# Performance work log

Measured on AMD Instinct MI355X. Metric: run time of the kernel, lower is better.

The kernel has to match this reference:

```python
import jax, jax.numpy as jnp
import numpy as np

N_NODES, N_EDGES, N_GRAPHS, EMB_DIM, IMG_DIM, N_TYPES = 50000, 800000, 64, 128, 4096, 30


def gcn_conv(x, W, b, row, col, ew, dis, n):
    # PyG GCNConv: x @ W.T, symmetric-normalized weighted aggregation with self-loops, + bias
    xw = x @ W.T                                            # [N, D]
    norm = dis[row] * ew * dis[col]                          # [E]
    agg = jax.ops.segment_sum(norm[:, None] * xw[row], col, num_segments=n)
    agg = agg + (dis * dis)[:, None] * xw                    # self-loop (weight 1) term
    return agg + b


def setup_inputs() -> dict:
    key = jax.random.key(0)
    ks = jax.random.split(key, 20)
    inp = {
        "images": jax.random.normal(ks[0], (N_GRAPHS, IMG_DIM), jnp.float32),
        "node_types": jax.random.randint(ks[1], (N_NODES,), 0, N_TYPES),
        "edge_index": jax.random.randint(ks[2], (2, N_EDGES), 0, N_NODES),
        "edge_attr": jax.random.uniform(ks[3], (N_EDGES,), jnp.float32),
        "batch": jnp.sort(jax.random.randint(ks[4], (N_NODES,), 0, N_GRAPHS)),
    }
    def lin(k, out_d, in_d):
        s = 1.0 / np.sqrt(in_d)
        kw, kb = jax.random.split(k)
        return (jax.random.uniform(kw, (out_d, in_d), jnp.float32, -s, s),
                jax.random.uniform(kb, (out_d,), jnp.float32, -s, s))
    inp["emb_table"] = jax.random.normal(ks[5], (N_TYPES, EMB_DIM), jnp.float32)
    inp["W_img"], inp["b_img"] = lin(ks[6], IMG_DIM, IMG_DIM)      # frozen image backbone head
    inp["W1"], inp["b1"] = lin(ks[7], EMB_DIM, EMB_DIM)
    inp["W2"], inp["b2"] = lin(ks[8], EMB_DIM, EMB_DIM)
    inp["W3"], inp["b3"] = lin(ks[9], EMB_DIM, EMB_DIM)
    inp["Wi"], inp["bi"] = lin(ks[10], EMB_DIM, IMG_DIM)
    inp["Wc"], inp["bc"] = lin(ks[11], EMB_DIM, IMG_DIM + EMB_DIM)
    return inp


def reference(images, node_types, edge_index, edge_attr, batch, emb_table,
              W_img, b_img, W1, b1, W2, b2, W3, b3, Wi, bi, Wc, bc):
    n = node_types.shape[0]
    B = images.shape[0]
    row, col = edge_index[0], edge_index[1]
    # gcn_norm with self-loops (fill value 1): deg at aggregation endpoint (col)
    deg = jax.ops.segment_sum(edge_attr, col, num_segments=n) + 1.0
    dis = jax.lax.rsqrt(deg)
    # frozen image model (linear stand-in for VGG fc head, output dim 4096)
    xi = images @ W_img.T + b_img                           # [B, 4096]
    # encode_images branch
    oi = xi @ Wi.T + bi
    oi = oi / jnp.linalg.norm(oi, axis=1, keepdims=True)
    # encode_images_with_graphs branch
    xg = emb_table[node_types]                              # [N, D]
    xg = jax.nn.relu(gcn_conv(xg, W1, b1, row, col, edge_attr, dis, n))
    xg = jax.nn.relu(gcn_conv(xg, W2, b2, row, col, edge_attr, dis, n))
    xg = gcn_conv(xg, W3, b3, row, col, edge_attr, dis, n)
    cnt = jax.ops.segment_sum(jnp.ones((n,), xg.dtype), batch, num_segments=B)
    pooled = jax.ops.segment_sum(xg, batch, num_segments=B) / jnp.maximum(cnt, 1.0)[:, None]
    oc = jnp.concatenate([xi, pooled], axis=1) @ Wc.T + bc
    oc = oc / jnp.linalg.norm(oc, axis=1, keepdims=True)
    return (oi, oc)
```

## Files before the change

kernel.cpp:

```cpp
#include <hip/hip_runtime.h>
#include <math.h>

#define NN 50000
#define NE 800000
#define NG 64
#define D 128
#define IMG 4096
#define NT 30
#define CAP 48

#define EBLK (NE / 256)
#define PBLK ((NT * D + 2 * D * 64) / 256)
#define CBLK (64 * IMG / 2 / 256)
#define GBLK ((NN + 63) / 64)
#define AGGBLK ((NN + 7) / 8)
#define KSPLIT 16
#define IMGHALF (64 * KSPLIT / 2)
#define IREDBLK (64 * IMG / 256)

typedef unsigned int uint;
typedef unsigned short ushort;
typedef __attribute__((ext_vector_type(8))) __bf16 bf16x8;
typedef __attribute__((ext_vector_type(4))) float f32x4;

__device__ __forceinline__ uint bf16rne(float f) {
  uint h = __float_as_uint(f);
  return (h + 0x7fffu + ((h >> 16) & 1u)) >> 16;
}
__device__ __forceinline__ uint pack2bf(float a, float b) {
  return bf16rne(a) | (bf16rne(b) << 16);
}
__device__ __forceinline__ float bflo(uint u) { return __uint_as_float(u << 16); }
__device__ __forceinline__ float bfhi(uint u) { return __uint_as_float(u & 0xffff0000u); }



__global__ __launch_bounds__(256) void setup_multi(
    const int* __restrict__ row, const int* __restrict__ col,
    const float* __restrict__ ew, int* __restrict__ cnt, float* __restrict__ degf,
    int2* __restrict__ ebuf,
    const float* __restrict__ emb, const float* __restrict__ W1, float* __restrict__ embW,
    const float* __restrict__ W2, const float* __restrict__ W3,
    uint* __restrict__ Wbf2, uint* __restrict__ Wbf3,
    const float* __restrict__ images, uint* __restrict__ imgAbf,
    const int* __restrict__ batch, int* __restrict__ goff) {
  int b = blockIdx.x;
  if (b < EBLK) {
    int e = b * 256 + threadIdx.x;
    if (e < NE) {
      int c = col[e];
      float wv = ew[e];
      int s = atomicAdd(&cnt[c], 1);
      atomicAdd(&degf[c], wv);
      if (s < CAP) ebuf[(size_t)c * CAP + s] = make_int2(row[e], __float_as_int(wv));
    }
  } else if (b < EBLK + PBLK) {
    int tid = (b - EBLK) * 256 + threadIdx.x;
    if (tid < NT * D) {
      int tt = tid >> 7, nn2 = tid & 127;
      const float* ep = emb + (size_t)tt * D;
      const float* wp = W1 + (size_t)nn2 * D;
      float acc = 0.f;
      for (int k = 0; k < D; k += 4) {
        float4 evv = *(const float4*)(ep + k);
        float4 wvv = *(const float4*)(wp + k);
        acc += evv.x * wvv.x + evv.y * wvv.y + evv.z * wvv.z + evv.w * wvv.w;
      }
      embW[tid] = acc;
    } else if (tid < NT * D + D * 64) {
      int j = tid - NT * D;
      float2 v = ((const float2*)W2)[j];
      Wbf2[j] = pack2bf(v.x, v.y);
    } else {
      int j = tid - NT * D - D * 64;
      float2 v = ((const float2*)W3)[j];
      Wbf3[j] = pack2bf(v.x, v.y);
    }
  } else if (b < EBLK + PBLK + CBLK) {
    int idx = (b - EBLK - PBLK) * 256 + threadIdx.x;
    float2 v = ((const float2*)images)[idx];
    imgAbf[idx] = pack2bf(v.x, v.y);
  } else {
    int g = threadIdx.x;
    if (g <= NG) {
      int lo = 0, hi = NN;
      while (lo < hi) {
        int mid = (lo + hi) >> 1;
        if (batch[mid] < g) lo = mid + 1; else hi = mid;
      }
      goff[g] = lo;
    }
  }
}


__global__ __launch_bounds__(256) void dis_kernel(const float* __restrict__ degf,
                                                  float* __restrict__ dis) {
  int i = blockIdx.x * 256 + threadIdx.x;
  if (i < NN) dis[i] = 1.0f / sqrtf(degf[i] + 1.0f);
}


__global__ __launch_bounds__(512) void lay1_fused(const int* __restrict__ cnt,
                                                  const int2* __restrict__ ebuf,
                                                  const float* __restrict__ dis,
                                                  const int* __restrict__ types,
                                                  const float* __restrict__ embW,
                                                  const float* __restrict__ b1,
                                                  uint* __restrict__ outbf) {
  __shared__ float sE[NT * D];
  __shared__ float sB[D];
  int t = threadIdx.x;
  for (int i = t; i < NT * D; i += 512) sE[i] = embW[i];
  if (t < D) sB[t] = b1[t];
  __syncthreads();
  int wave = t >> 6, lane = t & 63;
  #pragma unroll
  for (int r = 0; r < 4; r++) {
    int node = blockIdx.x * 32 + wave * 4 + r;
    if (node >= NN) continue;
    float ax = sB[2 * lane], ay = sB[2 * lane + 1];
    int n = min(cnt[node], CAP);
    int nc = (n + 7) >> 3;
    const int2* eb = ebuf + (size_t)node * CAP;
    float disc = dis[node];
    for (int c = 0; c < nc; c++) {
      const int2* ep = eb + (c << 3);
      int4 q0 = *(const int4*)(ep + 0);
      int4 q1 = *(const int4*)(ep + 2);
      int4 q2 = *(const int4*)(ep + 4);
      int4 q3 = *(const int4*)(ep + 6);
      int t0 = types[q0.x], t1 = types[q0.z], t2 = types[q1.x], t3 = types[q1.z];
      int t4 = types[q2.x], t5 = types[q2.z], t6 = types[q3.x], t7 = types[q3.z];
      float m0 = dis[q0.x] * __int_as_float(q0.y) * disc;
      float m1 = dis[q0.z] * __int_as_float(q0.w) * disc;
      float m2 = dis[q1.x] * __int_as_float(q1.y) * disc;
      float m3 = dis[q1.z] * __int_as_float(q1.w) * disc;
      float m4 = dis[q2.x] * __int_as_float(q2.y) * disc;
      float m5 = dis[q2.z] * __int_as_float(q2.w) * disc;
      float m6 = dis[q3.x] * __int_as_float(q3.y) * disc;
      float m7 = dis[q3.z] * __int_as_float(q3.w) * disc;
      float2 e0 = *(const float2*)&sE[t0 * D + 2 * lane];
      float2 e1 = *(const float2*)&sE[t1 * D + 2 * lane];
      float2 e2 = *(const float2*)&sE[t2 * D + 2 * lane];
      float2 e3 = *(const float2*)&sE[t3 * D + 2 * lane];
      float2 e4 = *(const float2*)&sE[t4 * D + 2 * lane];
      float2 e5 = *(const float2*)&sE[t5 * D + 2 * lane];
      float2 e6 = *(const float2*)&sE[t6 * D + 2 * lane];
      float2 e7 = *(const float2*)&sE[t7 * D + 2 * lane];
      ax = fmaf(m0, e0.x, ax); ay = fmaf(m0, e0.y, ay);
      ax = fmaf(m1, e1.x, ax); ay = fmaf(m1, e1.y, ay);
      ax = fmaf(m2, e2.x, ax); ay = fmaf(m2, e2.y, ay);
      ax = fmaf(m3, e3.x, ax); ay = fmaf(m3, e3.y, ay);
      ax = fmaf(m4, e4.x, ax); ay = fmaf(m4, e4.y, ay);
      ax = fmaf(m5, e5.x, ax); ay = fmaf(m5, e5.y, ay);
      ax = fmaf(m6, e6.x, ax); ay = fmaf(m6, e6.y, ay);
      ax = fmaf(m7, e7.x, ax); ay = fmaf(m7, e7.y, ay);
    }
    float dd = disc * disc;
    float2 es = *(const float2*)&sE[types[node] * D + 2 * lane];
    ax = fmaf(dd, es.x, ax);
    ay = fmaf(dd, es.y, ay);
    ax = fmaxf(ax, 0.f);
    ay = fmaxf(ay, 0.f);
    outbf[(size_t)node * 64 + lane] = pack2bf(ax, ay);
  }
}


__device__ __forceinline__ void node_gemm_body(const uint* __restrict__ Abf,
                                               const uint* __restrict__ Wbf,
                                               uint* __restrict__ outbf, int bx,
                                               ushort* __restrict__ tile) {
  int w = threadIdx.x >> 6, lane = threadIdx.x & 63;
  int quad = lane >> 4;
  int m0 = bx * 64 + w * 16;
  int mrow = m0 + (lane & 15);
  int arow = (mrow < NN) ? mrow : 0;
  uint4 afr[4];
  #pragma unroll
  for (int ks = 0; ks < 4; ks++)
    afr[ks] = *(const uint4*)(Abf + (size_t)arow * 64 + ks * 16 + quad * 4);
  f32x4 acc[8] = {};
  #pragma unroll
  for (int nt = 0; nt < 8; nt++) {
    int n = nt * 16 + (lane & 15);
    #pragma unroll
    for (int ks = 0; ks < 4; ks++) {
      union { uint4 u; bf16x8 v; } au, bu;
      au.u = afr[ks];
      bu.u = *(const uint4*)(Wbf + (size_t)n * 64 + ks * 16 + quad * 4);
      acc[nt] = __builtin_amdgcn_mfma_f32_16x16x32_bf16(au.v, bu.v, acc[nt], 0, 0, 0);
    }
  }
  ushort* tw = tile + w * 16 * 136;
  #pragma unroll
  for (int nt = 0; nt < 8; nt++)
    #pragma unroll
    for (int i = 0; i < 4; i++)
      tw[(quad * 4 + i) * 136 + nt * 16 + (lane & 15)] = (ushort)bf16rne(acc[nt][i]);
  __builtin_amdgcn_s_waitcnt(0);
  #pragma unroll
  for (int rep = 0; rep < 4; rep++) {
    int r = rep * 4 + quad;
    int j = lane & 15;
    int node = m0 + r;
    if (node < NN) {
      uint4 v = *(const uint4*)&tw[r * 136 + j * 8];
      *(uint4*)(outbf + (size_t)node * 64 + j * 4) = v;
    }
  }
}


__device__ __forceinline__ void img_mfma_body(const uint* __restrict__ Abf,
                                              const float* __restrict__ W,
                                              float* __restrict__ splitbuf, int bx, int by) {
  int wv = threadIdx.x >> 6, lane = threadIdx.x & 63;
  int quad = lane >> 4;
  int n = bx * 64 + wv * 16 + (lane & 15);
  int k0 = by * 256;
  f32x4 acc[4] = {{0.f, 0.f, 0.f, 0.f}, {0.f, 0.f, 0.f, 0.f},
                  {0.f, 0.f, 0.f, 0.f}, {0.f, 0.f, 0.f, 0.f}};
  const float* wp = W + (size_t)n * IMG + k0 + quad * 16;
  const uint* ap = Abf + (size_t)(lane & 15) * (IMG / 2) + k0 / 2 + quad * 8;
  #pragma unroll
  for (int ss = 0; ss < 4; ss++) {
    float4 w0 = *(const float4*)(wp + ss * 64);
    float4 w1 = *(const float4*)(wp + ss * 64 + 4);
    float4 w2 = *(const float4*)(wp + ss * 64 + 8);
    float4 w3 = *(const float4*)(wp + ss * 64 + 12);
    union { uint4 u; bf16x8 v; } b1u, b2u;
    b1u.u.x = pack2bf(w0.x, w0.y);
    b1u.u.y = pack2bf(w0.z, w0.w);
    b1u.u.z = pack2bf(w1.x, w1.y);
    b1u.u.w = pack2bf(w1.z, w1.w);
    b2u.u.x = pack2bf(w2.x, w2.y);
    b2u.u.y = pack2bf(w2.z, w2.w);
    b2u.u.z = pack2bf(w3.x, w3.y);
    b2u.u.w = pack2bf(w3.z, w3.w);
    #pragma unroll
    for (int mt = 0; mt < 4; mt++) {
      const uint* app = ap + (size_t)mt * 16 * (IMG / 2) + ss * 32;
      union { uint4 u; bf16x8 v; } a1u, a2u;
      a1u.u = *(const uint4*)(app);
      a2u.u = *(const uint4*)(app + 4);
      acc[mt] = __builtin_amdgcn_mfma_f32_16x16x32_bf16(a1u.v, b1u.v, acc[mt], 0, 0, 0);
      acc[mt] = __builtin_amdgcn_mfma_f32_16x16x32_bf16(a2u.v, b2u.v, acc[mt], 0, 0, 0);
    }
  }
  #pragma unroll
  for (int mt = 0; mt < 4; mt++)
    #pragma unroll
    for (int i = 0; i < 4; i++) {
      int m = mt * 16 + quad * 4 + i;
      splitbuf[((size_t)by * 64 + m) * IMG + n] = acc[mt][i];
    }
}


#define GA(k, s_) uint2 u##k = xw2[(size_t)(s_) * 32 + fl];
#define FA(k, m_) a0 = fmaf(m_, bflo(u##k.x), a0); a1 = fmaf(m_, bfhi(u##k.x), a1); \
                  a2 = fmaf(m_, bflo(u##k.y), a2); a3 = fmaf(m_, bfhi(u##k.y), a3);

__device__ __forceinline__ void aggregate2_body(const uint* __restrict__ xw,
                                                const int* __restrict__ cnt,
                                                const int2* __restrict__ ebuf,
                                                const float* __restrict__ dis,
                                                const float* __restrict__ bias, int relu,
                                                uint* __restrict__ outbf, int blk) {
  const uint2* xw2 = (const uint2*)xw;
  int wave = threadIdx.x >> 6;
  int lane = threadIdx.x & 63;
  int half = lane >> 5;
  int fl = lane & 31;
  int node = (blk * 4 + wave) * 2 + half;
  if (node >= NN) return;
  float a0 = 0.f, a1 = 0.f, a2 = 0.f, a3 = 0.f;
  int n = min(cnt[node], CAP);
  int nc = (n + 15) >> 4;
  const int2* eb = ebuf + (size_t)node * CAP;
  float disc = dis[node];
  for (int c = 0; c < nc; c++) {
    const int2* ep = eb + (c << 4);
    int4 r0 = *(const int4*)(ep + 0);
    int4 r1 = *(const int4*)(ep + 2);
    int4 r2 = *(const int4*)(ep + 4);
    int4 r3 = *(const int4*)(ep + 6);
    int4 r4 = *(const int4*)(ep + 8);
    int4 r5 = *(const int4*)(ep + 10);
    int4 r6 = *(const int4*)(ep + 12);
    int4 r7 = *(const int4*)(ep + 14);
    GA(0, r0.x)  GA(1, r0.z)  GA(2, r1.x)  GA(3, r1.z)
    GA(4, r2.x)  GA(5, r2.z)  GA(6, r3.x)  GA(7, r3.z)
    GA(8, r4.x)  GA(9, r4.z)  GA(10, r5.x) GA(11, r5.z)
    GA(12, r6.x) GA(13, r6.z) GA(14, r7.x) GA(15, r7.z)
    float m0 = dis[r0.x] * __int_as_float(r0.y) * disc;
    float m1 = dis[r0.z] * __int_as_float(r0.w) * disc;
    float m2 = dis[r1.x] * __int_as_float(r1.y) * disc;
    float m3 = dis[r1.z] * __int_as_float(r1.w) * disc;
    float m4 = dis[r2.x] * __int_as_float(r2.y) * disc;
    float m5 = dis[r2.z] * __int_as_float(r2.w) * disc;
    float m6 = dis[r3.x] * __int_as_float(r3.y) * disc;
    float m7 = dis[r3.z] * __int_as_float(r3.w) * disc;
    float m8 = dis[r4.x] * __int_as_float(r4.y) * disc;
    float m9 = dis[r4.z] * __int_as_float(r4.w) * disc;
    float m10 = dis[r5.x] * __int_as_float(r5.y) * disc;
    float m11 = dis[r5.z] * __int_as_float(r5.w) * disc;
    float m12 = dis[r6.x] * __int_as_float(r6.y) * disc;
    float m13 = dis[r6.z] * __int_as_float(r6.w) * disc;
    float m14 = dis[r7.x] * __int_as_float(r7.y) * disc;
    float m15 = dis[r7.z] * __int_as_float(r7.w) * disc;
    FA(0, m0)  FA(1, m1)  FA(2, m2)  FA(3, m3)
    FA(4, m4)  FA(5, m5)  FA(6, m6)  FA(7, m7)
    FA(8, m8)  FA(9, m9)  FA(10, m10) FA(11, m11)
    FA(12, m12) FA(13, m13) FA(14, m14) FA(15, m15)
  }
  float dd = disc * disc;
  {
    uint2 u = xw2[(size_t)node * 32 + fl];
    a0 = fmaf(dd, bflo(u.x), a0);
    a1 = fmaf(dd, bfhi(u.x), a1);
    a2 = fmaf(dd, bflo(u.y), a2);
    a3 = fmaf(dd, bfhi(u.y), a3);
  }
  float4 b = *(const float4*)(bias + 4 * fl);
  a0 += b.x; a1 += b.y; a2 += b.z; a3 += b.w;
  if (relu) {
    a0 = fmaxf(a0, 0.f);
    a1 = fmaxf(a1, 0.f);
    a2 = fmaxf(a2, 0.f);
    a3 = fmaxf(a3, 0.f);
  }
  uint2 o;
  o.x = pack2bf(a0, a1);
  o.y = pack2bf(a2, a3);
  ((uint2*)outbf)[(size_t)node * 32 + fl] = o;
}

__global__ __launch_bounds__(256) void gemm2_plus_img(const uint* __restrict__ bufX,
                                                      const uint* __restrict__ wbf2,
                                                      uint* __restrict__ bufB,
                                                      const uint* __restrict__ imgAbf,
                                                      const float* __restrict__ Wimg,
                                                      float* __restrict__ splitbuf) {
  __shared__ ushort tile[4 * 16 * 136];
  int b = blockIdx.x;
  if (b < IMGHALF) {
    img_mfma_body(imgAbf, Wimg, splitbuf, b & 63, b >> 6);
  } else {
    node_gemm_body(bufX, wbf2, bufB, b - IMGHALF, tile);
  }
}

__global__ __launch_bounds__(256) void agg2_plus_img(const uint* __restrict__ bufB,
                                                     const int* __restrict__ cnt,
                                                     const int2* __restrict__ ebuf,
                                                     const float* __restrict__ dis,
                                                     const float* __restrict__ b2,
                                                     uint* __restrict__ bufX,
                                                     const uint* __restrict__ imgAbf,
                                                     const float* __restrict__ Wimg,
                                                     float* __restrict__ splitbuf) {
  int b = blockIdx.x;
  if (b < IMGHALF) {
    img_mfma_body(imgAbf, Wimg, splitbuf, b & 63, 8 + (b >> 6));
  } else {
    aggregate2_body(bufB, cnt, ebuf, dis, b2, 1, bufX, b - IMGHALF);
  }
}

__global__ __launch_bounds__(256) void gemm3_plus_imgred(const uint* __restrict__ bufX,
                                                         const uint* __restrict__ wbf3,
                                                         uint* __restrict__ bufB,
                                                         const float* __restrict__ splitbuf,
                                                         const float* __restrict__ b_img,
                                                         float* __restrict__ xcat) {
  __shared__ ushort tile[4 * 16 * 136];
  int b = blockIdx.x;
  if (b < IREDBLK) {
    int idx = b * 256 + threadIdx.x;
    float acc = b_img[idx & (IMG - 1)];
    #pragma unroll
    for (int s = 0; s < KSPLIT; s++) acc += splitbuf[(size_t)s * 64 * IMG + idx];
    xcat[(size_t)(idx >> 12) * (IMG + D) + (idx & (IMG - 1))] = acc;
  } else {
    node_gemm_body(bufX, wbf3, bufB, b - IREDBLK, tile);
  }
}


__device__ __forceinline__ void gemm64_body(const float* __restrict__ A, int lda,
                                            const float* __restrict__ W,
                                            const float* __restrict__ bias,
                                            float* __restrict__ out, int N, int K,
                                            int kChunk, int bx, int by,
                                            float (*xs)[68], float (*ws)[68]) {
  int t = threadIdx.x;
  int n0 = bx * 64;
  int k0 = by * kChunk;
  int kEnd = min(K, k0 + kChunk);
  int tn = t & 15;
  int tm = t >> 4;
  float acc[4][4] = {};
  if (by == 0) {
    #pragma unroll
    for (int ni = 0; ni < 4; ni++) {
      float bv = bias[n0 + tn * 4 + ni];
      #pragma unroll
      for (int mi = 0; mi < 4; mi++) acc[mi][ni] = bv;
    }
  }
  for (int kt = k0; kt < kEnd; kt += 16) {
    int kc = (t & 3) * 4;
    int rr = t >> 2;
    float4 va = *(const float4*)(A + (size_t)rr * lda + kt + kc);
    xs[kc + 0][rr] = va.x; xs[kc + 1][rr] = va.y; xs[kc + 2][rr] = va.z; xs[kc + 3][rr] = va.w;
    float4 vw = *(const float4*)(W + (size_t)(n0 + rr) * K + kt + kc);
    ws[kc + 0][rr] = vw.x; ws[kc + 1][rr] = vw.y; ws[kc + 2][rr] = vw.z; ws[kc + 3][rr] = vw.w;
    __syncthreads();
    #pragma unroll
    for (int k = 0; k < 16; k++) {
      float4 xv = *(const float4*)&xs[k][tm * 4];
      float4 wv = *(const float4*)&ws[k][tn * 4];
      float xm[4] = {xv.x, xv.y, xv.z, xv.w};
      float wn[4] = {wv.x, wv.y, wv.z, wv.w};
      #pragma unroll
      for (int mi = 0; mi < 4; mi++)
        #pragma unroll
        for (int ni = 0; ni < 4; ni++)
          acc[mi][ni] = fmaf(xm[mi], wn[ni], acc[mi][ni]);
    }
    __syncthreads();
  }
  #pragma unroll
  for (int mi = 0; mi < 4; mi++)
    #pragma unroll
    for (int ni = 0; ni < 4; ni++)
      atomicAdd(&out[(size_t)(tm * 4 + mi) * N + n0 + tn * 4 + ni], acc[mi][ni]);
}

__global__ __launch_bounds__(256) void agg3_plus_oi(const uint* __restrict__ bufB,
                                                    const int* __restrict__ cnt,
                                                    const int2* __restrict__ ebuf,
                                                    const float* __restrict__ dis,
                                                    const float* __restrict__ b3,
                                                    uint* __restrict__ bufX,
                                                    const float* __restrict__ xcat,
                                                    const float* __restrict__ Wi,
                                                    const float* __restrict__ bi,
                                                    float* __restrict__ oi_raw) {
  __shared__ float xs[16][68];
  __shared__ float ws[16][68];
  int b = blockIdx.x;
  if (b < 64) {
    gemm64_body(xcat, IMG + D, Wi, bi, oi_raw, D, IMG, 128, b & 1, b >> 1, xs, ws);
  } else {
    aggregate2_body(bufB, cnt, ebuf, dis, b3, 0, bufX, b - 64);
  }
}


__global__ __launch_bounds__(64) void pool_bf(const uint* __restrict__ xb,
                                              const int* __restrict__ goff,
                                              float* __restrict__ xcat) {
  int g = blockIdx.x >> 5;
  int chunk = blockIdx.x & 31;
  int fl = threadIdx.x;
  int s = goff[g], e = goff[g + 1];
  float inv = 1.0f / fmaxf((float)(e - s), 1.0f);
  float ax = 0.f, ay = 0.f;
  for (int i = s + chunk; i < e; i += 32) {
    uint u = xb[(size_t)i * 64 + fl];
    ax += bflo(u);
    ay += bfhi(u);
  }
  atomicAdd(&xcat[(size_t)g * (IMG + D) + IMG + 2 * fl], ax * inv);
  atomicAdd(&xcat[(size_t)g * (IMG + D) + IMG + 2 * fl + 1], ay * inv);
}

__global__ __launch_bounds__(256) void gemm_oc(const float* __restrict__ xcat,
                                               const float* __restrict__ Wc,
                                               const float* __restrict__ bc,
                                               float* __restrict__ oc_raw) {
  __shared__ float xs[16][68];
  __shared__ float ws[16][68];
  int b = blockIdx.x;
  gemm64_body(xcat, IMG + D, Wc, bc, oc_raw, D, IMG + D, 176, b & 1, b >> 1, xs, ws);
}

__global__ __launch_bounds__(128) void normalize_rows(const float* __restrict__ oi_raw,
                                                      const float* __restrict__ oc_raw,
                                                      float* __restrict__ out) {
  int r = blockIdx.x;
  int t = threadIdx.x;
  const float* src = (r < 64) ? (oi_raw + r * D) : (oc_raw + (r - 64) * D);
  float v = src[t];
  __shared__ float red[128];
  red[t] = v * v;
  __syncthreads();
  for (int s = 64; s > 0; s >>= 1) {
    if (t < s) red[t] += red[t + s];
    __syncthreads();
  }
  out[r * D + t] = v / sqrtf(red[0]);
}


extern "C" void kernel_launch(void* const* d_in, const int* in_sizes, int n_in,
                              void* d_out, int out_size, void* d_ws, size_t ws_size,
                              hipStream_t stream) {
  const float* images = (const float*)d_in[0];
  const int* node_types = (const int*)d_in[1];
  const int* erow = (const int*)d_in[2];
  const int* ecol = erow + NE;
  const float* eattr = (const float*)d_in[3];
  const int* batch = (const int*)d_in[4];
  const float* emb = (const float*)d_in[5];
  const float* W_img = (const float*)d_in[6];
  const float* b_img = (const float*)d_in[7];
  const float* W1 = (const float*)d_in[8];
  const float* b1 = (const float*)d_in[9];
  const float* W2 = (const float*)d_in[10];
  const float* b2 = (const float*)d_in[11];
  const float* W3 = (const float*)d_in[12];
  const float* b3 = (const float*)d_in[13];
  const float* Wi = (const float*)d_in[14];
  const float* bi = (const float*)d_in[15];
  const float* Wc = (const float*)d_in[16];
  const float* bc = (const float*)d_in[17];
  float* out = (float*)d_out;

  char* w = (char*)d_ws;
  auto alloc = [&](size_t bytes) -> void* {
    void* p = (void*)w;
    w += (bytes + 511) & ~(size_t)511;
    return p;
  };
  int* cnt = (int*)alloc((size_t)NN * 4);
  float* degf = (float*)alloc((size_t)NN * 4);
  float* xcat = (float*)alloc((size_t)64 * (IMG + D) * 4);
  float* oi_raw = (float*)alloc(64 * D * 4);
  float* oc_raw = (float*)alloc(64 * D * 4);
  int2* ebuf = (int2*)alloc((size_t)NN * CAP * 8);
  size_t zero_bytes = (size_t)(w - (char*)d_ws);
  int* goff = (int*)alloc((NG + 1) * 4);
  float* dis = (float*)alloc(NN * 4);
  float* embW1 = (float*)alloc(NT * D * 4);
  uint* wbf2 = (uint*)alloc(D * 64 * 4);
  uint* wbf3 = (uint*)alloc(D * 64 * 4);
  uint* bufX = (uint*)alloc((size_t)NN * D * 2);
  uint* bufB = (uint*)alloc((size_t)NN * D * 2);
  uint* imgAbf = (uint*)alloc((size_t)64 * IMG * 2);
  float* splitbuf = (float*)alloc((size_t)KSPLIT * 64 * IMG * 4);

  hipMemsetAsync(d_ws, 0, zero_bytes, stream);

  setup_multi<<<EBLK + PBLK + CBLK + 1, 256, 0, stream>>>(
      erow, ecol, eattr, cnt, degf, ebuf, emb, W1, embW1, W2, W3, wbf2, wbf3,
      images, imgAbf, batch, goff);
  dis_kernel<<<(NN + 255) / 256, 256, 0, stream>>>(degf, dis);
  lay1_fused<<<(NN + 31) / 32, 512, 0, stream>>>(cnt, ebuf, dis, node_types, embW1, b1, bufX);
  gemm2_plus_img<<<IMGHALF + GBLK, 256, 0, stream>>>(bufX, wbf2, bufB, imgAbf, W_img,
                                                     splitbuf);
  agg2_plus_img<<<IMGHALF + AGGBLK, 256, 0, stream>>>(bufB, cnt, ebuf, dis, b2, bufX,
                                                      imgAbf, W_img, splitbuf);
  gemm3_plus_imgred<<<IREDBLK + GBLK, 256, 0, stream>>>(bufX, wbf3, bufB, splitbuf, b_img,
                                                        xcat);
  agg3_plus_oi<<<64 + AGGBLK, 256, 0, stream>>>(bufB, cnt, ebuf, dis, b3, bufX,
                                                xcat, Wi, bi, oi_raw);
  pool_bf<<<NG * 32, 64, 0, stream>>>(bufX, goff, xcat);
  gemm_oc<<<48, 256, 0, stream>>>(xcat, Wc, bc, oc_raw);
  normalize_rows<<<128, 128, 0, stream>>>(oi_raw, oc_raw, out);
}
```

Measured before the change: 443.3 us.

## Reschedule image GEMM into setup kernel and split oc GEMM across stages

The whole image-head split-K GEMM now runs inside the first setup kernel, reading fp32 images directly and packing to bf16 in registers, so the separate image-cast pass and the split across two later kernels go away. The float degree atomics are dropped and degrees are instead recomputed per node from the bucketed edge buffer in a new dis kernel. Work is reshuffled so the image reduction overlaps layer-2 GEMM, the oi GEMM overlaps layer-3 GEMM, and the image part of the oc GEMM overlaps layer-3 aggregation, leaving only the pooled columns for a tiny tail kernel. The cost is that aggregation 2 now runs alone, the setup kernel becomes heavier, and the degree sum only sees the first CAP edges per node.

```diff
diff --git a/kernel.cpp b/kernel.cpp
--- a/kernel.cpp
+++ b/kernel.cpp
@@ -11,11 +11,10 @@
 
 #define EBLK (NE / 256)
 #define PBLK ((NT * D + 2 * D * 64) / 256)
-#define CBLK (64 * IMG / 2 / 256)
 #define GBLK ((NN + 63) / 64)
 #define AGGBLK ((NN + 7) / 8)
 #define KSPLIT 16
-#define IMGHALF (64 * KSPLIT / 2)
+#define IMGALL (64 * KSPLIT)
 #define IREDBLK (64 * IMG / 256)
 
 typedef unsigned int uint;
@@ -35,27 +34,83 @@
 
 
 
-__global__ __launch_bounds__(256) void setup_multi(
+__device__ __forceinline__ void img_mfma_body(const float* __restrict__ A,
+                                              const float* __restrict__ W,
+                                              float* __restrict__ splitbuf, int bx, int by) {
+  int wv = threadIdx.x >> 6, lane = threadIdx.x & 63;
+  int quad = lane >> 4;
+  int n = bx * 64 + wv * 16 + (lane & 15);
+  int k0 = by * 256;
+  f32x4 acc[4] = {{0.f, 0.f, 0.f, 0.f}, {0.f, 0.f, 0.f, 0.f},
+                  {0.f, 0.f, 0.f, 0.f}, {0.f, 0.f, 0.f, 0.f}};
+  const float* wp = W + (size_t)n * IMG + k0 + quad * 16;
+  const float* ap = A + (size_t)(lane & 15) * IMG + k0 + quad * 16;
+  #pragma unroll
+  for (int ss = 0; ss < 4; ss++) {
+    float4 w0 = *(const float4*)(wp + ss * 64);
+    float4 w1 = *(const float4*)(wp + ss * 64 + 4);
+    float4 w2 = *(const float4*)(wp + ss * 64 + 8);
+    float4 w3 = *(const float4*)(wp + ss * 64 + 12);
+    union { uint4 u; bf16x8 v; } b1u, b2u;
+    b1u.u.x = pack2bf(w0.x, w0.y);
+    b1u.u.y = pack2bf(w0.z, w0.w);
+    b1u.u.z = pack2bf(w1.x, w1.y);
+    b1u.u.w = pack2bf(w1.z, w1.w);
+    b2u.u.x = pack2bf(w2.x, w2.y);
+    b2u.u.y = pack2bf(w2.z, w2.w);
+    b2u.u.z = pack2bf(w3.x, w3.y);
+    b2u.u.w = pack2bf(w3.z, w3.w);
+    #pragma unroll
+    for (int mt = 0; mt < 4; mt++) {
+      const float* app = ap + (size_t)mt * 16 * IMG + ss * 64;
+      float4 a0_ = *(const float4*)(app);
+      float4 a1_ = *(const float4*)(app + 4);
+      float4 a2_ = *(const float4*)(app + 8);
+      float4 a3_ = *(const float4*)(app + 12);
+      union { uint4 u; bf16x8 v; } a1u, a2u;
+      a1u.u.x = pack2bf(a0_.x, a0_.y);
+      a1u.u.y = pack2bf(a0_.z, a0_.w);
+      a1u.u.z = pack2bf(a1_.x, a1_.y);
+      a1u.u.w = pack2bf(a1_.z, a1_.w);
+      a2u.u.x = pack2bf(a2_.x, a2_.y);
+      a2u.u.y = pack2bf(a2_.z, a2_.w);
+      a2u.u.z = pack2bf(a3_.x, a3_.y);
+      a2u.u.w = pack2bf(a3_.z, a3_.w);
+      acc[mt] = __builtin_amdgcn_mfma_f32_16x16x32_bf16(a1u.v, b1u.v, acc[mt], 0, 0, 0);
+      acc[mt] = __builtin_amdgcn_mfma_f32_16x16x32_bf16(a2u.v, b2u.v, acc[mt], 0, 0, 0);
+    }
+  }
+  #pragma unroll
+  for (int mt = 0; mt < 4; mt++)
+    #pragma unroll
+    for (int i = 0; i < 4; i++) {
+      int m = mt * 16 + quad * 4 + i;
+      splitbuf[((size_t)by * 64 + m) * IMG + n] = acc[mt][i];
+    }
+}
+
+
+__global__ __launch_bounds__(256) void setup_fused(
     const int* __restrict__ row, const int* __restrict__ col,
-    const float* __restrict__ ew, int* __restrict__ cnt, float* __restrict__ degf,
-    int2* __restrict__ ebuf,
+    const float* __restrict__ ew, int* __restrict__ cnt, int2* __restrict__ ebuf,
     const float* __restrict__ emb, const float* __restrict__ W1, float* __restrict__ embW,
     const float* __restrict__ W2, const float* __restrict__ W3,
     uint* __restrict__ Wbf2, uint* __restrict__ Wbf3,
-    const float* __restrict__ images, uint* __restrict__ imgAbf,
+    const float* __restrict__ images, const float* __restrict__ Wimg,
+    float* __restrict__ splitbuf,
     const int* __restrict__ batch, int* __restrict__ goff) {
   int b = blockIdx.x;
-  if (b < EBLK) {
-    int e = b * 256 + threadIdx.x;
+  if (b < IMGALL) {
+    img_mfma_body(images, Wimg, splitbuf, b & 63, b >> 6);
+  } else if (b < IMGALL + EBLK) {
+    int e = (b - IMGALL) * 256 + threadIdx.x;
     if (e < NE) {
       int c = col[e];
-      float wv = ew[e];
       int s = atomicAdd(&cnt[c], 1);
-      atomicAdd(&degf[c], wv);
-      if (s < CAP) ebuf[(size_t)c * CAP + s] = make_int2(row[e], __float_as_int(wv));
-    }
-  } else if (b < EBLK + PBLK) {
-    int tid = (b - EBLK) * 256 + threadIdx.x;
+      if (s < CAP) ebuf[(size_t)c * CAP + s] = make_int2(row[e], __float_as_int(ew[e]));
+    }
+  } else if (b < IMGALL + EBLK + PBLK) {
+    int tid = (b - IMGALL - EBLK) * 256 + threadIdx.x;
     if (tid < NT * D) {
       int tt = tid >> 7, nn2 = tid & 127;
       const float* ep = emb + (size_t)tt * D;
@@ -76,10 +131,6 @@
       float2 v = ((const float2*)W3)[j];
       Wbf3[j] = pack2bf(v.x, v.y);
     }
-  } else if (b < EBLK + PBLK + CBLK) {
-    int idx = (b - EBLK - PBLK) * 256 + threadIdx.x;
-    float2 v = ((const float2*)images)[idx];
-    imgAbf[idx] = pack2bf(v.x, v.y);
   } else {
     int g = threadIdx.x;
     if (g <= NG) {
@@ -94,10 +145,21 @@
 }
 
 
-__global__ __launch_bounds__(256) void dis_kernel(const float* __restrict__ degf,
-                                                  float* __restrict__ dis) {
-  int i = blockIdx.x * 256 + threadIdx.x;
-  if (i < NN) dis[i] = 1.0f / sqrtf(degf[i] + 1.0f);
+__global__ __launch_bounds__(256) void node_dis(const int2* __restrict__ ebuf,
+                                                float* __restrict__ dis) {
+  int lane = threadIdx.x & 63;
+  int sub = lane >> 4, fl = lane & 15;
+  int node = (blockIdx.x * 4 + (threadIdx.x >> 6)) * 4 + sub;
+  if (node >= NN) return;
+  const int2* eb = ebuf + (size_t)node * CAP;
+  float acc = 0.f;
+  #pragma unroll
+  for (int j = 0; j < CAP / 16; j++) acc += __int_as_float(eb[fl + j * 16].y);
+  acc += __shfl_xor(acc, 8);
+  acc += __shfl_xor(acc, 4);
+  acc += __shfl_xor(acc, 2);
+  acc += __shfl_xor(acc, 1);
+  if (fl == 0) dis[node] = 1.0f / sqrtf(acc + 1.0f);
 }
 
 
@@ -210,52 +272,6 @@
       *(uint4*)(outbf + (size_t)node * 64 + j * 4) = v;
     }
   }
-}
-
-
-__device__ __forceinline__ void img_mfma_body(const uint* __restrict__ Abf,
-                                              const float* __restrict__ W,
-                                              float* __restrict__ splitbuf, int bx, int by) {
-  int wv = threadIdx.x >> 6, lane = threadIdx.x & 63;
-  int quad = lane >> 4;
-  int n = bx * 64 + wv * 16 + (lane & 15);
-  int k0 = by * 256;
-  f32x4 acc[4] = {{0.f, 0.f, 0.f, 0.f}, {0.f, 0.f, 0.f, 0.f},
-                  {0.f, 0.f, 0.f, 0.f}, {0.f, 0.f, 0.f, 0.f}};
-  const float* wp = W + (size_t)n * IMG + k0 + quad * 16;
-  const uint* ap = Abf + (size_t)(lane & 15) * (IMG / 2) + k0 / 2 + quad * 8;
-  #pragma unroll
-  for (int ss = 0; ss < 4; ss++) {
-    float4 w0 = *(const float4*)(wp + ss * 64);
-    float4 w1 = *(const float4*)(wp + ss * 64 + 4);
-    float4 w2 = *(const float4*)(wp + ss * 64 + 8);
-    float4 w3 = *(const float4*)(wp + ss * 64 + 12);
-    union { uint4 u; bf16x8 v; } b1u, b2u;
-    b1u.u.x = pack2bf(w0.x, w0.y);
-    b1u.u.y = pack2bf(w0.z, w0.w);
-    b1u.u.z = pack2bf(w1.x, w1.y);
-    b1u.u.w = pack2bf(w1.z, w1.w);
-    b2u.u.x = pack2bf(w2.x, w2.y);
-    b2u.u.y = pack2bf(w2.z, w2.w);
-    b2u.u.z = pack2bf(w3.x, w3.y);
-    b2u.u.w = pack2bf(w3.z, w3.w);
-    #pragma unroll
-    for (int mt = 0; mt < 4; mt++) {
-      const uint* app = ap + (size_t)mt * 16 * (IMG / 2) + ss * 32;
-      union { uint4 u; bf16x8 v; } a1u, a2u;
-      a1u.u = *(const uint4*)(app);
-      a2u.u = *(const uint4*)(app + 4);
-      acc[mt] = __builtin_amdgcn_mfma_f32_16x16x32_bf16(a1u.v, b1u.v, acc[mt], 0, 0, 0);
-      acc[mt] = __builtin_amdgcn_mfma_f32_16x16x32_bf16(a2u.v, b2u.v, acc[mt], 0, 0, 0);
-    }
-  }
-  #pragma unroll
-  for (int mt = 0; mt < 4; mt++)
-    #pragma unroll
-    for (int i = 0; i < 4; i++) {
-      int m = mt * 16 + quad * 4 + i;
-      splitbuf[((size_t)by * 64 + m) * IMG + n] = acc[mt][i];
-    }
 }
 
 
@@ -338,57 +354,6 @@
   ((uint2*)outbf)[(size_t)node * 32 + fl] = o;
 }
 
-__global__ __launch_bounds__(256) void gemm2_plus_img(const uint* __restrict__ bufX,
-                                                      const uint* __restrict__ wbf2,
-                                                      uint* __restrict__ bufB,
-                                                      const uint* __restrict__ imgAbf,
-                                                      const float* __restrict__ Wimg,
-                                                      float* __restrict__ splitbuf) {
-  __shared__ ushort tile[4 * 16 * 136];
-  int b = blockIdx.x;
-  if (b < IMGHALF) {
-    img_mfma_body(imgAbf, Wimg, splitbuf, b & 63, b >> 6);
-  } else {
-    node_gemm_body(bufX, wbf2, bufB, b - IMGHALF, tile);
-  }
-}
-
-__global__ __launch_bounds__(256) void agg2_plus_img(const uint* __restrict__ bufB,
-                                                     const int* __restrict__ cnt,
-                                                     const int2* __restrict__ ebuf,
-                                                     const float* __restrict__ dis,
-                                                     const float* __restrict__ b2,
-                                                     uint* __restrict__ bufX,
-                                                     const uint* __restrict__ imgAbf,
-                                                     const float* __restrict__ Wimg,
-                                                     float* __restrict__ splitbuf) {
-  int b = blockIdx.x;
-  if (b < IMGHALF) {
-    img_mfma_body(imgAbf, Wimg, splitbuf, b & 63, 8 + (b >> 6));
-  } else {
-    aggregate2_body(bufB, cnt, ebuf, dis, b2, 1, bufX, b - IMGHALF);
-  }
-}
-
-__global__ __launch_bounds__(256) void gemm3_plus_imgred(const uint* __restrict__ bufX,
-                                                         const uint* __restrict__ wbf3,
-                                                         uint* __restrict__ bufB,
-                                                         const float* __restrict__ splitbuf,
-                                                         const float* __restrict__ b_img,
-                                                         float* __restrict__ xcat) {
-  __shared__ ushort tile[4 * 16 * 136];
-  int b = blockIdx.x;
-  if (b < IREDBLK) {
-    int idx = b * 256 + threadIdx.x;
-    float acc = b_img[idx & (IMG - 1)];
-    #pragma unroll
-    for (int s = 0; s < KSPLIT; s++) acc += splitbuf[(size_t)s * 64 * IMG + idx];
-    xcat[(size_t)(idx >> 12) * (IMG + D) + (idx & (IMG - 1))] = acc;
-  } else {
-    node_gemm_body(bufX, wbf3, bufB, b - IREDBLK, tile);
-  }
-}
-
 
 __device__ __forceinline__ void gemm64_body(const float* __restrict__ A, int lda,
                                             const float* __restrict__ W,
@@ -440,21 +405,67 @@
       atomicAdd(&out[(size_t)(tm * 4 + mi) * N + n0 + tn * 4 + ni], acc[mi][ni]);
 }
 
-__global__ __launch_bounds__(256) void agg3_plus_oi(const uint* __restrict__ bufB,
-                                                    const int* __restrict__ cnt,
-                                                    const int2* __restrict__ ebuf,
-                                                    const float* __restrict__ dis,
-                                                    const float* __restrict__ b3,
-                                                    uint* __restrict__ bufX,
-                                                    const float* __restrict__ xcat,
-                                                    const float* __restrict__ Wi,
-                                                    const float* __restrict__ bi,
-                                                    float* __restrict__ oi_raw) {
+__global__ __launch_bounds__(256) void gemm2_plus_imgred(const uint* __restrict__ bufX,
+                                                         const uint* __restrict__ wbf2,
+                                                         uint* __restrict__ bufB,
+                                                         const float* __restrict__ splitbuf,
+                                                         const float* __restrict__ b_img,
+                                                         float* __restrict__ xcat) {
+  __shared__ ushort tile[4 * 16 * 136];
+  int b = blockIdx.x;
+  if (b < IREDBLK) {
+    int idx = b * 256 + threadIdx.x;
+    float acc = b_img[idx & (IMG - 1)];
+    #pragma unroll
+    for (int s = 0; s < KSPLIT; s++) acc += splitbuf[(size_t)s * 64 * IMG + idx];
+    xcat[(size_t)(idx >> 12) * (IMG + D) + (idx & (IMG - 1))] = acc;
+  } else {
+    node_gemm_body(bufX, wbf2, bufB, b - IREDBLK, tile);
+  }
+}
+
+__global__ __launch_bounds__(256) void aggregate2(const uint* __restrict__ xw,
+                                                  const int* __restrict__ cnt,
+                                                  const int2* __restrict__ ebuf,
+                                                  const float* __restrict__ dis,
+                                                  const float* __restrict__ bias, int relu,
+                                                  uint* __restrict__ outbf) {
+  aggregate2_body(xw, cnt, ebuf, dis, bias, relu, outbf, blockIdx.x);
+}
+
+__global__ __launch_bounds__(256) void gemm3_plus_oi(const uint* __restrict__ bufX,
+                                                     const uint* __restrict__ wbf3,
+                                                     uint* __restrict__ bufB,
+                                                     const float* __restrict__ xcat,
+                                                     const float* __restrict__ Wi,
+                                                     const float* __restrict__ bi,
+                                                     float* __restrict__ oi_raw) {
+  __shared__ __align__(16) char smem[4 * 16 * 136 * 2];
+  int b = blockIdx.x;
+  if (b < 64) {
+    float (*xs)[68] = (float(*)[68])smem;
+    float (*ws)[68] = (float(*)[68])(smem + 16 * 68 * 4);
+    gemm64_body(xcat, IMG + D, Wi, bi, oi_raw, D, IMG, 128, b & 1, b >> 1, xs, ws);
+  } else {
+    node_gemm_body(bufX, wbf3, bufB, b - 64, (ushort*)smem);
+  }
+}
+
+__global__ __launch_bounds__(256) void agg3_plus_ocmain(const uint* __restrict__ bufB,
+                                                        const int* __restrict__ cnt,
+                                                        const int2* __restrict__ ebuf,
+                                                        const float* __restrict__ dis,
+                                                        const float* __restrict__ b3,
+                                                        uint* __restrict__ bufX,
+                                                        const float* __restrict__ xcat,
+                                                        const float* __restrict__ Wc,
+                                                        const float* __restrict__ bc,
+                                                        float* __restrict__ oc_raw) {
   __shared__ float xs[16][68];
   __shared__ float ws[16][68];
   int b = blockIdx.x;
   if (b < 64) {
-    gemm64_body(xcat, IMG + D, Wi, bi, oi_raw, D, IMG, 128, b & 1, b >> 1, xs, ws);
+    gemm64_body(xcat, IMG + D, Wc, bc, oc_raw, D, IMG + D, 128, b & 1, b >> 1, xs, ws);
   } else {
     aggregate2_body(bufB, cnt, ebuf, dis, b3, 0, bufX, b - 64);
   }
@@ -479,14 +490,13 @@
   atomicAdd(&xcat[(size_t)g * (IMG + D) + IMG + 2 * fl + 1], ay * inv);
 }
 
-__global__ __launch_bounds__(256) void gemm_oc(const float* __restrict__ xcat,
+__global__ __launch_bounds__(256) void oc_tail(const float* __restrict__ xcat,
                                                const float* __restrict__ Wc,
                                                const float* __restrict__ bc,
                                                float* __restrict__ oc_raw) {
   __shared__ float xs[16][68];
   __shared__ float ws[16][68];
-  int b = blockIdx.x;
-  gemm64_body(xcat, IMG + D, Wc, bc, oc_raw, D, IMG + D, 176, b & 1, b >> 1, xs, ws);
+  gemm64_body(xcat, IMG + D, Wc, bc, oc_raw, D, IMG + D, 4096, blockIdx.x, 1, xs, ws);
 }
 
 __global__ __launch_bounds__(128) void normalize_rows(const float* __restrict__ oi_raw,
@@ -538,7 +548,6 @@
     return p;
   };
   int* cnt = (int*)alloc((size_t)NN * 4);
-  float* degf = (float*)alloc((size_t)NN * 4);
   float* xcat = (float*)alloc((size_t)64 * (IMG + D) * 4);
   float* oi_raw = (float*)alloc(64 * D * 4);
   float* oc_raw = (float*)alloc(64 * D * 4);
@@ -551,25 +560,22 @@
   uint* wbf3 = (uint*)alloc(D * 64 * 4);
   uint* bufX = (uint*)alloc((size_t)NN * D * 2);
   uint* bufB = (uint*)alloc((size_t)NN * D * 2);
-  uint* imgAbf = (uint*)alloc((size_t)64 * IMG * 2);
   float* splitbuf = (float*)alloc((size_t)KSPLIT * 64 * IMG * 4);
 
   hipMemsetAsync(d_ws, 0, zero_bytes, stream);
 
-  setup_multi<<<EBLK + PBLK + CBLK + 1, 256, 0, stream>>>(
-      erow, ecol, eattr, cnt, degf, ebuf, emb, W1, embW1, W2, W3, wbf2, wbf3,
-      images, imgAbf, batch, goff);
-  dis_kernel<<<(NN + 255) / 256, 256, 0, stream>>>(degf, dis);
+  setup_fused<<<IMGALL + EBLK + PBLK + 1, 256, 0, stream>>>(
+      erow, ecol, eattr, cnt, ebuf, emb, W1, embW1, W2, W3, wbf2, wbf3,
+      images, W_img, splitbuf, batch, goff);
+  node_dis<<<(NN + 15) / 16, 256, 0, stream>>>(ebuf, dis);
   lay1_fused<<<(NN + 31) / 32, 512, 0, stream>>>(cnt, ebuf, dis, node_types, embW1, b1, bufX);
-  gemm2_plus_img<<<IMGHALF + GBLK, 256, 0, stream>>>(bufX, wbf2, bufB, imgAbf, W_img,
-                                                     splitbuf);
-  agg2_plus_img<<<IMGHALF + AGGBLK, 256, 0, stream>>>(bufB, cnt, ebuf, dis, b2, bufX,
-                                                      imgAbf, W_img, splitbuf);
-  gemm3_plus_imgred<<<IREDBLK + GBLK, 256, 0, stream>>>(bufX, wbf3, bufB, splitbuf, b_img,
+  gemm2_plus_imgred<<<IREDBLK + GBLK, 256, 0, stream>>>(bufX, wbf2, bufB, splitbuf, b_img,
                                                         xcat);
-  agg3_plus_oi<<<64 + AGGBLK, 256, 0, stream>>>(bufB, cnt, ebuf, dis, b3, bufX,
-                                                xcat, Wi, bi, oi_raw);
+  aggregate2<<<AGGBLK, 256, 0, stream>>>(bufB, cnt, ebuf, dis, b2, 1, bufX);
+  gemm3_plus_oi<<<64 + GBLK, 256, 0, stream>>>(bufX, wbf3, bufB, xcat, Wi, bi, oi_raw);
+  agg3_plus_ocmain<<<64 + AGGBLK, 256, 0, stream>>>(bufB, cnt, ebuf, dis, b3, bufX,
+                                                    xcat, Wc, bc, oc_raw);
   pool_bf<<<NG * 32, 64, 0, stream>>>(bufX, goff, xcat);
-  gemm_oc<<<48, 256, 0, stream>>>(xcat, Wc, bc, oc_raw);
+  oc_tail<<<2, 256, 0, stream>>>(xcat, Wc, bc, oc_raw);
   normalize_rows<<<128, 128, 0, stream>>>(oi_raw, oc_raw, out);
 }
```

Result: faster. 410.3 us (-7.4%).
